# Optimization experiments

Hardware: AMD Instinct MI355X
Metric: run time of the kernel (lower is better)

Reference implementation:

```python
import jax, jax.numpy as jnp
import numpy as np

NUM_STAGES = 8
NUM_CODEBOOKS = 1024  # 2**10
DATA_DIM = 256
T = 131072


def setup_inputs() -> dict:
    key = jax.random.key(0)
    k_x, k_cb = jax.random.split(key)
    input_data = jax.random.normal(k_x, (T, DATA_DIM), dtype=jnp.float32)
    # torch init: Uniform(-1/K, 1/K) per stage
    bound = 1.0 / NUM_CODEBOOKS
    codebooks = jax.random.uniform(
        k_cb, (NUM_STAGES, NUM_CODEBOOKS, DATA_DIM), dtype=jnp.float32,
        minval=-bound, maxval=bound)
    return {"input_data": input_data, "codebooks": codebooks}


def _hard_vq(residual, cb):
    dists = (jnp.sum(residual * residual, axis=1, keepdims=True)
             - 2.0 * (residual @ cb.T)
             + jnp.sum(cb * cb, axis=1)[None, :])
    idx = jnp.argmin(dists, axis=1)          # [T]
    q = cb[idx]                               # gather -> [T, D]
    return q, residual - q, idx


def reference(input_data, codebooks):
    # eval path: stage_map=None (mask of ones), train_mode=False
    residual = input_data
    recon = jnp.zeros_like(input_data)
    mses = []
    for i in range(codebooks.shape[0]):  # fixed small stage loop
        q, residual, _ = _hard_vq(residual, codebooks[i])
        recon = recon + q  # intermediate reconstruction = cumulative sum of q
        mses.append(jnp.mean((recon - input_data) ** 2))
    final_output = recon
    return final_output, jnp.stack(mses)
```

## Files before the change

### kernel.cpp

```cpp
#include <hip/hip_runtime.h>
#include <stdint.h>


#define T_ROWS   131072
#define DIM      256
#define NSTAGE   8
#define NCB      1024
#define WROWS    32
#define NWAVE    4
#define BLK_ROWS (NWAVE * WROWS)
#define NTHREADS 256
#define CHUNK_CW 32
#define NCHUNK   (NCB / CHUNK_CW)
#define NGCH     (NSTAGE * NCHUNK)
#define CHUNK_BYTES (CHUNK_CW * 512)

#define WS_B_BYTES     (NSTAGE * NCB * 512)
#define WS_CNORM_OFF   WS_B_BYTES
#define WS_CNORM_BYTES (NSTAGE * NCB * 4)
#define WS_MSE_OFF     (WS_CNORM_OFF + WS_CNORM_BYTES)
#define WS_IDX_OFF     (WS_MSE_OFF + 64)

typedef __attribute__((ext_vector_type(8)))  short  s16x8;
typedef __attribute__((ext_vector_type(8)))  __bf16 bf16x8;
typedef __attribute__((ext_vector_type(4)))  float  f32x4;
typedef __attribute__((ext_vector_type(16))) float  f32x16;

__device__ __forceinline__ unsigned short f2bf(float f) {
  union { float f; unsigned u; } v; v.f = f;
  unsigned r = v.u + 0x7FFFu + ((v.u >> 16) & 1u);
  return (unsigned short)(r >> 16);
}

__global__ void vq_prep(const float* __restrict__ CB, char* __restrict__ wsb,
                        float* __restrict__ cnorm) {
  const int tid = threadIdx.x;
  const int b   = blockIdx.x;
  {
    const int g   = b >> 2;
    const int s0q = (b & 3) * 4;
    const int c32 = tid & 31;
    const int sh  = tid >> 5;
    const int s   = s0q + (sh >> 1);
    const int hi  = sh & 1;
    const int cw  = g * 32 + c32;
    const float* src = CB + (size_t)cw * DIM + 16 * s + 8 * hi;
    f32x4 a = *(const f32x4*)(src);
    f32x4 c = *(const f32x4*)(src + 4);
    s16x8 h;
#pragma unroll
    for (int e = 0; e < 4; ++e) { h[e] = (short)f2bf(a[e]); h[4 + e] = (short)f2bf(c[e]); }
    *(s16x8*)(wsb + (size_t)g * 16384 + s * 1024 + hi * 512 + c32 * 16) = h;
  }
  {
    const int cwl = tid >> 5;
    const int j   = tid & 31;
    const int cw  = b * 8 + cwl;
    const float* src = CB + (size_t)cw * DIM + 8 * j;
    f32x4 a = *(const f32x4*)(src);
    f32x4 c = *(const f32x4*)(src + 4);
    float sq = a[0]*a[0] + a[1]*a[1] + a[2]*a[2] + a[3]*a[3]
             + c[0]*c[0] + c[1]*c[1] + c[2]*c[2] + c[3]*c[3];
#pragma unroll
    for (int m = 1; m <= 16; m <<= 1) sq += __shfl_xor(sq, m);
    if (j == 0) cnorm[cw] = sq;
  }
}

__global__ __launch_bounds__(NTHREADS, 4)
void vq_search(const float* __restrict__ X,
               const char* __restrict__ wsb, const float* __restrict__ cnorm,
               unsigned short* __restrict__ IDX, float* __restrict__ wsmse) {
  __shared__ __align__(16) char  lds_cb[2][CHUNK_BYTES];
  __shared__ unsigned short lds_idx[BLK_ROWS];
  __shared__ float lds_n[BLK_ROWS];
  __shared__ float lds_msum[NWAVE];

  const int tid  = threadIdx.x;
  const int wave = tid >> 6;
  const int lane = tid & 63;
  const int c32  = lane & 31;
  const int hi   = lane >> 5;

  const int rowbase = blockIdx.x * BLK_ROWS + wave * WROWS;

  bf16x8 af[16];
  {
    const float* px = X + (size_t)(rowbase + c32) * DIM + 8 * hi;
    float s2 = 0.f;
#pragma unroll
    for (int s = 0; s < 16; ++s) {
      f32x4 a = *(const f32x4*)(px + 16 * s);
      f32x4 b = *(const f32x4*)(px + 16 * s + 4);
      bf16x8 tt;
#pragma unroll
      for (int e = 0; e < 4; ++e) {
        tt[e] = (__bf16)a[e]; tt[4 + e] = (__bf16)b[e];
        s2 += a[e] * a[e] + b[e] * b[e];
      }
      af[s] = tt;
    }
    float v = s2 + __shfl_xor(s2, 32);
    if (lane < 32) lds_n[wave * WROWS + c32] = v;
  }

#pragma unroll
  for (int i = 0; i < 4; ++i) {
    const int seg = (wave * 4 + i) * 1024;
    __builtin_amdgcn_global_load_lds(
        (const __attribute__((address_space(1))) char*)(wsb + seg + lane * 16),
        (__attribute__((address_space(3))) char*)(&lds_cb[0][0] + seg),
        16, 0, 0);
  }
  asm volatile("s_waitcnt vmcnt(0)" ::: "memory");
  __builtin_amdgcn_sched_barrier(0);

#pragma unroll 1
  for (int st = 0; st < NSTAGE; ++st) {
    float mv[16];
#pragma unroll
    for (int r = 0; r < 16; ++r) mv[r] = -3.402823466e38f;

#pragma unroll 1
    for (int ch = 0; ch < NCHUNK; ++ch) {
      const int gf = st * NCHUNK + ch;

      __builtin_amdgcn_sched_barrier(0);
      __builtin_amdgcn_s_barrier();
      __builtin_amdgcn_sched_barrier(0);

      if (gf + 1 < NGCH) {
        const char* src = wsb + (size_t)(gf + 1) * CHUNK_BYTES;
        char* dst = &lds_cb[(gf + 1) & 1][0];
#pragma unroll
        for (int i = 0; i < 4; ++i) {
          const int seg = (wave * 4 + i) * 1024;
          __builtin_amdgcn_global_load_lds(
              (const __attribute__((address_space(1))) char*)(src + seg + lane * 16),
              (__attribute__((address_space(3))) char*)(dst + seg),
              16, 0, 0);
        }
      }

      const float cnv = cnorm[gf * CHUNK_CW + c32];

      f32x16 acc;
#pragma unroll
      for (int r = 0; r < 16; ++r) acc[r] = 0.f;

      const char* buf = &lds_cb[gf & 1][0] + lane * 16;
      __builtin_amdgcn_s_setprio(1);
#pragma unroll
      for (int s = 0; s < 16; ++s) {
        bf16x8 b = *(const bf16x8*)(buf + s * 1024);
        acc = __builtin_amdgcn_mfma_f32_32x32x16_bf16(af[s], b, acc, 0, 0, 0);
      }
      __builtin_amdgcn_s_setprio(0);

      const float cnh = 0.5f * cnv;
      const unsigned col = (unsigned)(ch * CHUNK_CW + c32);
#pragma unroll
      for (int r = 0; r < 16; ++r) {
        union { float f; unsigned u; } p;
        p.f = acc[r] - cnh;
        p.u = (p.u & 0xFFFFFC00u) | col;
        mv[r] = fmaxf(mv[r], p.f);
      }

      asm volatile("s_waitcnt vmcnt(0)" ::: "memory");
      __builtin_amdgcn_sched_barrier(0);
    }

    float msum = 0.f;
#pragma unroll
    for (int r = 0; r < 16; ++r) {
      float v = mv[r];
#pragma unroll
      for (int m = 1; m <= 16; m <<= 1) v = fmaxf(v, __shfl_xor(v, m));
      union { float f; unsigned u; } w; w.f = v;
      const float vtrue = __builtin_bit_cast(float, w.u & 0xFFFFFC00u);
      const int   row   = (r & 3) + 8 * (r >> 2) + 4 * hi;
      const int   wrow  = wave * WROWS + row;
      const float n_new = lds_n[wrow] - 2.0f * vtrue;
      msum += n_new;
      if (c32 == 0) {
        lds_n[wrow]   = n_new;
        const int ix = (int)(w.u & 1023u);
        lds_idx[wrow] = (unsigned short)ix;
        IDX[st * T_ROWS + rowbase + row] = (unsigned short)ix;
      }
    }
    msum += __shfl_xor(msum, 32);
    if (lane == 0) lds_msum[wave] = msum;

    if (st != NSTAGE - 1) {
      const int idx = (int)lds_idx[wave * WROWS + c32];
      const char* q = wsb + (size_t)st * NCB * 512
                    + (size_t)(idx >> 5) * 16384 + hi * 512 + (idx & 31) * 16;
#pragma unroll
      for (int s = 0; s < 16; ++s) {
        bf16x8 qb = *(const bf16x8*)(q + s * 1024);
        bf16x8 tt = af[s];
#pragma unroll
        for (int e = 0; e < 8; ++e)
          tt[e] = (__bf16)((float)tt[e] - (float)qb[e]);
        af[s] = tt;
      }
    }

    __builtin_amdgcn_s_barrier();

    if (wave == 0) {
      float v = (lane < NWAVE) ? lds_msum[lane] : 0.f;
      v += __shfl_xor(v, 1);
      v += __shfl_xor(v, 2);
      if (lane == 0) atomicAdd(wsmse + st, v);
    }
  }
}

__global__ __launch_bounds__(256)
void vq_recon(const char* __restrict__ wsb, const unsigned short* __restrict__ IDX,
              float* __restrict__ OUT) {
  const int tid = threadIdx.x;
  const int row = blockIdx.x * (256 / 8) + (tid >> 3);
  const int g   = tid & 7;

  int idxs[NSTAGE];
#pragma unroll
  for (int st = 0; st < NSTAGE; ++st) idxs[st] = IDX[st * T_ROWS + row];

  float a[32];
#pragma unroll
  for (int d = 0; d < 32; ++d) a[d] = 0.f;

#pragma unroll
  for (int st = 0; st < NSTAGE; ++st) {
    const char* q = wsb + (size_t)st * NCB * 512
                  + (size_t)(idxs[st] >> 5) * 16384 + (idxs[st] & 31) * 16;
#pragma unroll
    for (int k = 0; k < 4; ++k) {
      const int s  = 2 * g + (k >> 1);
      const int h2 = (k & 1);
      bf16x8 qb = *(const bf16x8*)(q + s * 1024 + h2 * 512);
#pragma unroll
      for (int e = 0; e < 8; ++e) a[k * 8 + e] += (float)qb[e];
    }
  }

  float* po = OUT + (size_t)row * DIM + g * 32;
#pragma unroll
  for (int m = 0; m < 8; ++m) {
    f32x4 o = {a[4 * m], a[4 * m + 1], a[4 * m + 2], a[4 * m + 3]};
    *(f32x4*)(po + 4 * m) = o;
  }
}

__global__ void vq_fin(const float* __restrict__ wsmse, float* __restrict__ OUT) {
  const int i = threadIdx.x;
  if (i < NSTAGE) {
    OUT[(size_t)T_ROWS * DIM + i] = wsmse[i] * (1.0f / ((float)T_ROWS * (float)DIM));
  }
}

extern "C" void kernel_launch(void* const* d_in, const int* in_sizes, int n_in,
                              void* d_out, int out_size, void* d_ws, size_t ws_size,
                              hipStream_t stream) {
  (void)in_sizes; (void)n_in; (void)out_size; (void)ws_size;
  const float* X  = (const float*)d_in[0];
  const float* CB = (const float*)d_in[1];
  float* OUT = (float*)d_out;
  char*  wsb   = (char*)d_ws;
  float* cnorm = (float*)((char*)d_ws + WS_CNORM_OFF);
  float* wsmse = (float*)((char*)d_ws + WS_MSE_OFF);
  unsigned short* IDX = (unsigned short*)((char*)d_ws + WS_IDX_OFF);

  hipMemsetAsync(wsmse, 0, NSTAGE * sizeof(float), stream);
  hipLaunchKernelGGL(vq_prep, dim3(1024), dim3(256), 0, stream,
                     CB, wsb, cnorm);
  hipLaunchKernelGGL(vq_search, dim3(T_ROWS / BLK_ROWS), dim3(NTHREADS), 0, stream,
                     X, wsb, cnorm, IDX, wsmse);
  hipLaunchKernelGGL(vq_recon, dim3(T_ROWS / (256 / 8)), dim3(256), 0, stream,
                     wsb, IDX, OUT);
  hipLaunchKernelGGL(vq_fin, dim3(1), dim3(64), 0, stream, wsmse, OUT);
}
```

Measured before the change: 804.8 us.

## Process 64 rows per wave with two MFMA tiles sharing each codebook fragment

Each wave now holds two 32-row input tiles and issues two MFMAs per codebook fragment read from LDS. Blocks shrink to 2 waves, so a block still covers 128 rows and the grid size is unchanged. The goal is to halve LDS reads and barrier overhead per MFMA, since each B fragment is reused across 64 rows. In exchange each wave needs twice the registers for inputs and accumulators, which lowers occupancy (launch bounds drop to 2) and leaves fewer waves to hide latency.

```diff
diff --git a/kernel.cpp b/kernel.cpp
--- a/kernel.cpp
+++ b/kernel.cpp
@@ -6,10 +6,10 @@
 #define DIM      256
 #define NSTAGE   8
 #define NCB      1024
-#define WROWS    32
-#define NWAVE    4
+#define WROWS    64
+#define NWAVE    2
 #define BLK_ROWS (NWAVE * WROWS)
-#define NTHREADS 256
+#define NTHREADS (NWAVE * 64)
 #define CHUNK_CW 32
 #define NCHUNK   (NCB / CHUNK_CW)
 #define NGCH     (NSTAGE * NCHUNK)
@@ -67,7 +67,7 @@
   }
 }
 
-__global__ __launch_bounds__(NTHREADS, 4)
+__global__ __launch_bounds__(NTHREADS, 2)
 void vq_search(const float* __restrict__ X,
                const char* __restrict__ wsb, const float* __restrict__ cnorm,
                unsigned short* __restrict__ IDX, float* __restrict__ wsmse) {
@@ -84,9 +84,10 @@
 
   const int rowbase = blockIdx.x * BLK_ROWS + wave * WROWS;
 
-  bf16x8 af[16];
-  {
-    const float* px = X + (size_t)(rowbase + c32) * DIM + 8 * hi;
+  bf16x8 af[2][16];
+#pragma unroll
+  for (int t = 0; t < 2; ++t) {
+    const float* px = X + (size_t)(rowbase + t * 32 + c32) * DIM + 8 * hi;
     float s2 = 0.f;
 #pragma unroll
     for (int s = 0; s < 16; ++s) {
@@ -98,15 +99,15 @@
         tt[e] = (__bf16)a[e]; tt[4 + e] = (__bf16)b[e];
         s2 += a[e] * a[e] + b[e] * b[e];
       }
-      af[s] = tt;
+      af[t][s] = tt;
     }
     float v = s2 + __shfl_xor(s2, 32);
-    if (lane < 32) lds_n[wave * WROWS + c32] = v;
-  }
-
-#pragma unroll
-  for (int i = 0; i < 4; ++i) {
-    const int seg = (wave * 4 + i) * 1024;
+    if (lane < 32) lds_n[wave * WROWS + t * 32 + c32] = v;
+  }
+
+#pragma unroll
+  for (int i = 0; i < 8; ++i) {
+    const int seg = (wave * 8 + i) * 1024;
     __builtin_amdgcn_global_load_lds(
         (const __attribute__((address_space(1))) char*)(wsb + seg + lane * 16),
         (__attribute__((address_space(3))) char*)(&lds_cb[0][0] + seg),
@@ -117,9 +118,11 @@
 
 #pragma unroll 1
   for (int st = 0; st < NSTAGE; ++st) {
-    float mv[16];
-#pragma unroll
-    for (int r = 0; r < 16; ++r) mv[r] = -3.402823466e38f;
+    float mv[2][16];
+#pragma unroll
+    for (int t = 0; t < 2; ++t)
+#pragma unroll
+      for (int r = 0; r < 16; ++r) mv[t][r] = -3.402823466e38f;
 
 #pragma unroll 1
     for (int ch = 0; ch < NCHUNK; ++ch) {
@@ -133,8 +136,8 @@
         const char* src = wsb + (size_t)(gf + 1) * CHUNK_BYTES;
         char* dst = &lds_cb[(gf + 1) & 1][0];
 #pragma unroll
-        for (int i = 0; i < 4; ++i) {
-          const int seg = (wave * 4 + i) * 1024;
+        for (int i = 0; i < 8; ++i) {
+          const int seg = (wave * 8 + i) * 1024;
           __builtin_amdgcn_global_load_lds(
               (const __attribute__((address_space(1))) char*)(src + seg + lane * 16),
               (__attribute__((address_space(3))) char*)(dst + seg),
@@ -144,16 +147,17 @@
 
       const float cnv = cnorm[gf * CHUNK_CW + c32];
 
-      f32x16 acc;
-#pragma unroll
-      for (int r = 0; r < 16; ++r) acc[r] = 0.f;
+      f32x16 acc0, acc1;
+#pragma unroll
+      for (int r = 0; r < 16; ++r) { acc0[r] = 0.f; acc1[r] = 0.f; }
 
       const char* buf = &lds_cb[gf & 1][0] + lane * 16;
       __builtin_amdgcn_s_setprio(1);
 #pragma unroll
       for (int s = 0; s < 16; ++s) {
         bf16x8 b = *(const bf16x8*)(buf + s * 1024);
-        acc = __builtin_amdgcn_mfma_f32_32x32x16_bf16(af[s], b, acc, 0, 0, 0);
+        acc0 = __builtin_amdgcn_mfma_f32_32x32x16_bf16(af[0][s], b, acc0, 0, 0, 0);
+        acc1 = __builtin_amdgcn_mfma_f32_32x32x16_bf16(af[1][s], b, acc1, 0, 0, 0);
       }
       __builtin_amdgcn_s_setprio(0);
 
@@ -161,10 +165,11 @@
       const unsigned col = (unsigned)(ch * CHUNK_CW + c32);
 #pragma unroll
       for (int r = 0; r < 16; ++r) {
-        union { float f; unsigned u; } p;
-        p.f = acc[r] - cnh;
-        p.u = (p.u & 0xFFFFFC00u) | col;
-        mv[r] = fmaxf(mv[r], p.f);
+        union { float f; unsigned u; } p0, p1;
+        p0.f = acc0[r] - cnh; p0.u = (p0.u & 0xFFFFFC00u) | col;
+        p1.f = acc1[r] - cnh; p1.u = (p1.u & 0xFFFFFC00u) | col;
+        mv[0][r] = fmaxf(mv[0][r], p0.f);
+        mv[1][r] = fmaxf(mv[1][r], p1.f);
       }
 
       asm volatile("s_waitcnt vmcnt(0)" ::: "memory");
@@ -173,38 +178,43 @@
 
     float msum = 0.f;
 #pragma unroll
-    for (int r = 0; r < 16; ++r) {
-      float v = mv[r];
-#pragma unroll
-      for (int m = 1; m <= 16; m <<= 1) v = fmaxf(v, __shfl_xor(v, m));
-      union { float f; unsigned u; } w; w.f = v;
-      const float vtrue = __builtin_bit_cast(float, w.u & 0xFFFFFC00u);
-      const int   row   = (r & 3) + 8 * (r >> 2) + 4 * hi;
-      const int   wrow  = wave * WROWS + row;
-      const float n_new = lds_n[wrow] - 2.0f * vtrue;
-      msum += n_new;
-      if (c32 == 0) {
-        lds_n[wrow]   = n_new;
-        const int ix = (int)(w.u & 1023u);
-        lds_idx[wrow] = (unsigned short)ix;
-        IDX[st * T_ROWS + rowbase + row] = (unsigned short)ix;
-      }
-    }
+    for (int t = 0; t < 2; ++t)
+#pragma unroll
+      for (int r = 0; r < 16; ++r) {
+        float v = mv[t][r];
+#pragma unroll
+        for (int m = 1; m <= 16; m <<= 1) v = fmaxf(v, __shfl_xor(v, m));
+        union { float f; unsigned u; } w; w.f = v;
+        const float vtrue = __builtin_bit_cast(float, w.u & 0xFFFFFC00u);
+        const int   row   = t * 32 + (r & 3) + 8 * (r >> 2) + 4 * hi;
+        const int   wrow  = wave * WROWS + row;
+        const float n_new = lds_n[wrow] - 2.0f * vtrue;
+        msum += n_new;
+        if (c32 == 0) {
+          lds_n[wrow]   = n_new;
+          const int ix = (int)(w.u & 1023u);
+          lds_idx[wrow] = (unsigned short)ix;
+          IDX[st * T_ROWS + rowbase + row] = (unsigned short)ix;
+        }
+      }
     msum += __shfl_xor(msum, 32);
     if (lane == 0) lds_msum[wave] = msum;
 
     if (st != NSTAGE - 1) {
-      const int idx = (int)lds_idx[wave * WROWS + c32];
-      const char* q = wsb + (size_t)st * NCB * 512
-                    + (size_t)(idx >> 5) * 16384 + hi * 512 + (idx & 31) * 16;
-#pragma unroll
-      for (int s = 0; s < 16; ++s) {
-        bf16x8 qb = *(const bf16x8*)(q + s * 1024);
-        bf16x8 tt = af[s];
-#pragma unroll
-        for (int e = 0; e < 8; ++e)
-          tt[e] = (__bf16)((float)tt[e] - (float)qb[e]);
-        af[s] = tt;
+#pragma unroll
+      for (int t = 0; t < 2; ++t) {
+        const int idx = (int)lds_idx[wave * WROWS + t * 32 + c32];
+        const char* q = wsb + (size_t)st * NCB * 512
+                      + (size_t)(idx >> 5) * 16384 + hi * 512 + (idx & 31) * 16;
+#pragma unroll
+        for (int s = 0; s < 16; ++s) {
+          bf16x8 qb = *(const bf16x8*)(q + s * 1024);
+          bf16x8 tt = af[t][s];
+#pragma unroll
+          for (int e = 0; e < 8; ++e)
+            tt[e] = (__bf16)((float)tt[e] - (float)qb[e]);
+          af[t][s] = tt;
+        }
       }
     }
 
@@ -213,7 +223,6 @@
     if (wave == 0) {
       float v = (lane < NWAVE) ? lds_msum[lane] : 0.f;
       v += __shfl_xor(v, 1);
-      v += __shfl_xor(v, 2);
       if (lane == 0) atomicAdd(wsmse + st, v);
     }
   }
```

New measurement: 813.4 us. No clear change (+1.1%).
